# Optimization experiments

Hardware: AMD Instinct MI355X
Metric: run time of the kernel (lower is better)

The kernel has to match this reference:

```python
import jax, jax.numpy as jnp
import numpy as np

N_ORDER = 64
PRED_LEN = 720
SEQ_LEN = 720
ENC_IN = 321
BATCH = 16


def _hippo_legs(N):
    # HiPPO-LegS continuous transition (A, B), float64 numpy
    q = np.arange(N, dtype=np.float64)
    col, row = np.meshgrid(q, q)
    r = 2.0 * q + 1.0
    M = -(np.where(row >= col, r, 0.0) - np.diag(q))
    T = np.sqrt(np.diag(2.0 * q + 1.0))
    A = T @ M @ np.linalg.inv(T)
    B = np.diag(T)[:, None].copy()
    return A, B


def _discretize_bilinear(A, B, dt):
    # scipy.signal.cont2discrete(..., method='bilinear') equivalent
    N = A.shape[0]
    I = np.eye(N)
    BL = np.linalg.inv(I - (dt / 2.0) * A)
    Ad = BL @ (I + (dt / 2.0) * A)
    Bd = (BL @ (dt * B)).squeeze(-1)
    return Ad, Bd


def _legendre_eval_matrix(N, dt):
    # ss.eval_legendre(np.arange(N)[:,None], 1 - 2*vals).T via 3-term recurrence
    vals = np.arange(0.0, 1.0, dt)
    x = 1.0 - 2.0 * vals
    Ps = [np.ones_like(x), x]
    for n in range(1, N - 1):
        Ps.append(((2.0 * n + 1.0) * x * Ps[-1] - n * Ps[-2]) / (n + 1.0))
    return np.stack(Ps[:N], axis=0).T  # [len(vals), N]


def setup_inputs() -> dict:
    key = jax.random.key(0)
    k1, k2, k3 = jax.random.split(key, 3)
    dt = 1.0 / PRED_LEN
    A, B = _hippo_legs(N_ORDER)
    Ad, Bd = _discretize_bilinear(A, B, dt)
    eval_matrix = _legendre_eval_matrix(N_ORDER, dt)
    bound = 1.0 / np.sqrt(N_ORDER)  # torch nn.Linear default init range
    return {
        "x_enc": jax.random.normal(k1, (BATCH, SEQ_LEN, ENC_IN), dtype=jnp.float32),
        "A": jnp.asarray(Ad, dtype=jnp.float32),
        "B_vec": jnp.asarray(Bd, dtype=jnp.float32),
        "eval_matrix": jnp.asarray(eval_matrix, dtype=jnp.float32),
        "W_mlp": jax.random.uniform(k2, (N_ORDER, N_ORDER), jnp.float32, -bound, bound),
        "b_mlp": jax.random.uniform(k3, (N_ORDER,), jnp.float32, -bound, bound),
        "affine_weight": jnp.ones((1, 1, ENC_IN), jnp.float32),
        "affine_bias": jnp.zeros((1, 1, ENC_IN), jnp.float32),
    }


def reference(x_enc, A, B_vec, eval_matrix, W_mlp, b_mlp, affine_weight, affine_bias):
    P, N = eval_matrix.shape  # pred_len, proj_degree

    # RevIN-style instance normalization (means/stdev detached in torch)
    means = jax.lax.stop_gradient(jnp.mean(x_enc, axis=1, keepdims=True))
    x = x_enc - means
    stdev = jax.lax.stop_gradient(jnp.sqrt(jnp.var(x, axis=1, keepdims=True) + 1e-5))
    x = x / stdev
    x = x * affine_weight + affine_bias

    x_in = x[:, -P:]                         # [B, P, E]
    xs = jnp.transpose(x_in, (1, 0, 2))      # [P, B, E]: time-major for scan
    c0 = jnp.zeros((x_in.shape[0], x_in.shape[2], N), x_enc.dtype)

    def step(c, f):
        # c_t = c_{t-1} @ A^T + f_t B  (HiPPO-LegS linear recurrence)
        c_new = c @ A.T + f[..., None] * B_vec
        return c_new, c_new

    _, cs = jax.lax.scan(step, c0, xs)       # [P, B, E, N]

    out1 = cs @ W_mlp.T + b_mlp              # mlp over coefficient dim N
    x_dec_c = out1[P - 1]                    # [B, E, N] (seq_len >= pred_len branch)
    x_dec = x_dec_c @ eval_matrix.T          # [B, E, P] Legendre reconstruction
    x_dec = jnp.transpose(x_dec, (0, 2, 1))  # [B, P, E]

    # de-normalize
    x_dec = (x_dec - affine_bias) / (affine_weight + 1e-10)
    x_dec = x_dec * stdev + means
    return x_dec
```

## Files before the change

kernel.cpp:

```cpp
#include <hip/hip_runtime.h>
#include <math.h>

#define BATCH 16
#define SEQ   720
#define ENC   321
#define ENCP  324
#define NORD  64
#define PRED  720
#define NPAIR (BATCH*ENC)

#define WS_MEAN   0
#define WS_STDEV  (WS_MEAN + NPAIR)
#define WS_KT     (WS_STDEV + NPAIR)
#define WS_EWT    (WS_KT + PRED*NORD)
#define WS_EVB    (WS_EWT + NORD*PRED)
#define WS_C      (WS_EVB + PRED)
#define WS_A64    (WS_C + BATCH*NORD*ENCP)

#define GB_G      0
#define GB_PS_SUM 1572864
#define GB_PS_SS  (GB_PS_SUM + 24576)

__global__ __launch_bounds__(1024) void prep(const float* __restrict__ evalm,
        const float* __restrict__ W, const float* __restrict__ bm,
        const float* __restrict__ A, const float* __restrict__ Bv,
        float* __restrict__ ws)
{
    extern __shared__ float dsm[];
    const int tid  = threadIdx.x;
    const int lane = tid & 63;
    const int wv   = tid >> 6;
    if (blockIdx.x < 12) {
        float* smW = dsm;
        float* Et  = dsm + 64*65;
        const int r = blockIdx.x;
        for (int idx = tid; idx < 64*64; idx += 1024)
            smW[(idx>>6)*65 + (idx&63)] = W[idx];
        __syncthreads();
        float bv = bm[lane];
        #pragma unroll
        for (int k = 0; k < 4; k++) {
            int row = wv + k*16;
            if (row < 60) {
                int tp = r*60 + row;
                const float* ev = evalm + (size_t)tp*64;
                float acc = 0.f;
                #pragma unroll
                for (int kk = 0; kk < 16; kk++) {
                    float4 e4 = *(const float4*)&ev[4*kk];
                    acc += e4.x*smW[(4*kk+0)*65+lane] + e4.y*smW[(4*kk+1)*65+lane]
                         + e4.z*smW[(4*kk+2)*65+lane] + e4.w*smW[(4*kk+3)*65+lane];
                }
                Et[lane*61 + row] = acc;
                float pv = ev[lane] * bv;
                #pragma unroll
                for (int o = 32; o > 0; o >>= 1) pv += __shfl_down(pv, o);
                if (lane == 0) ws[WS_EVB + tp] = pv;
            }
        }
        __syncthreads();
        #pragma unroll
        for (int k = 0; k < 4; k++) {
            int idx = k*1024 + tid;
            int m = idx >> 6, row = idx & 63;
            if (row < 60)
                ws[WS_EWT + (size_t)m*720 + r*60 + row] = Et[m*61 + row];
        }
    } else {
        float* Kl  = dsm;
        float* Ap  = dsm + 4096;
        float* ApT = Ap + 64*68;
        float* Kt  = ws + WS_KT;
        for (int idx = tid; idx < 4096; idx += 1024) {
            int n = idx >> 6, m = idx & 63;
            float v = A[idx];
            Ap[n*68+m] = v; ApT[m*68+n] = v;
        }
        if (tid < 64) {
            float bv = Bv[tid];
            Kl[tid] = bv;
            Kt[(size_t)719*64 + tid] = bv;
        }
        __syncthreads();
        float ar[64];
        #pragma unroll
        for (int k = 0; k < 16; k++) {
            float4 v = *(const float4*)&Ap[lane*68 + 4*k];
            ar[4*k]=v.x; ar[4*k+1]=v.y; ar[4*k+2]=v.z; ar[4*k+3]=v.w;
        }
        for (int mm = 1; mm <= 32; mm <<= 1) {
            for (int j2 = mm + wv; j2 < 2*mm; j2 += 16) {
                const float* src = &Kl[(j2 - mm)*64];
                float acc = 0.f;
                #pragma unroll
                for (int k = 0; k < 16; k++) {
                    float4 s = *(const float4*)&src[4*k];
                    acc += ar[4*k]*s.x + ar[4*k+1]*s.y + ar[4*k+2]*s.z + ar[4*k+3]*s.w;
                }
                Kl[j2*64 + lane] = acc;
                Kt[(size_t)(719 - j2)*64 + lane] = acc;
            }
            float nacc[4];
            #pragma unroll
            for (int q = 0; q < 4; q++) {
                int c = wv*4 + q;
                const float* src = &ApT[c*68];
                float acc = 0.f;
                #pragma unroll
                for (int k = 0; k < 16; k++) {
                    float4 s = *(const float4*)&src[4*k];
                    acc += ar[4*k]*s.x + ar[4*k+1]*s.y + ar[4*k+2]*s.z + ar[4*k+3]*s.w;
                }
                nacc[q] = acc;
            }
            __syncthreads();
            #pragma unroll
            for (int q = 0; q < 4; q++) {
                int c = wv*4 + q;
                Ap[lane*68 + c]  = nacc[q];
                ApT[c*68 + lane] = nacc[q];
            }
            __syncthreads();
            #pragma unroll
            for (int k = 0; k < 16; k++) {
                float4 v = *(const float4*)&Ap[lane*68 + 4*k];
                ar[4*k]=v.x; ar[4*k+1]=v.y; ar[4*k+2]=v.z; ar[4*k+3]=v.w;
            }
        }
        for (int idx = tid; idx < 4096; idx += 1024)
            ws[WS_A64 + idx] = Ap[(idx>>6)*68 + (idx&63)];
    }
}

__global__ __launch_bounds__(256) void p2(float* __restrict__ ws)
{
    __shared__ float sv[4][64];
    const int lane = threadIdx.x & 63;
    const int wv   = threadIdx.x >> 6;
    const int r    = blockIdx.x*4 + wv;
    const float* A64 = ws + WS_A64;
    float* Kt = ws + WS_KT;
    float ar64[64];
    #pragma unroll
    for (int k = 0; k < 16; k++) {
        float4 v = *(const float4*)&A64[lane*64 + 4*k];
        ar64[4*k]=v.x; ar64[4*k+1]=v.y; ar64[4*k+2]=v.z; ar64[4*k+3]=v.w;
    }
    sv[wv][lane] = Kt[(size_t)(719 - r)*64 + lane];
    for (int j = r + 64; j <= 719; j += 64) {
        float acc = 0.f;
        #pragma unroll
        for (int k = 0; k < 16; k++) {
            float4 v = *(const float4*)&sv[wv][4*k];
            acc += ar64[4*k]*v.x + ar64[4*k+1]*v.y + ar64[4*k+2]*v.z + ar64[4*k+3]*v.w;
        }
        sv[wv][lane] = acc;
        Kt[(size_t)(719 - j)*64 + lane] = acc;
    }
}

__device__ inline float4 ldx(const float* __restrict__ x, int b, int t, int e4)
{
    float4 r = make_float4(0.f,0.f,0.f,0.f);
    const float* p = x + ((size_t)b*SEQ + t)*ENC;
    if (e4 + 3 < ENC) r = *(const float4*)&p[e4];
    else {
        if (e4   < ENC) r.x = p[e4];
        if (e4+1 < ENC) r.y = p[e4+1];
        if (e4+2 < ENC) r.z = p[e4+2];
    }
    return r;
}

__global__ __launch_bounds__(256) void k2(const float* __restrict__ x,
        float* __restrict__ gbuf, const float* __restrict__ ws)
{
    __shared__ float xt[2][12*64];
    __shared__ float ks[2][12*64];
    __shared__ float redn[12*64];
    __shared__ float reds[12*64];
    const int tid = threadIdx.x;
    const int bid = blockIdx.x;
    const int b = bid / 24, rem = bid % 24;
    const int et = rem / 4, tsp = rem % 4;
    const int e0 = et*64, t0 = tsp*180;

    const bool xon = tid < 192;
    const bool kon = tid >= 64;
    const int sx_t  = tid >> 4;
    const int sx_e4 = (tid & 15) * 4;
    const int sk    = tid - 64;
    const int sk_t  = sk >> 4;
    const int sk_m4 = (sk & 15) * 4;

    const float* Kt = ws + WS_KT;
    float s0=0,s1=0,s2=0,s3=0, q0=0,q1=0,q2=0,q3=0;
    float4 rx = make_float4(0,0,0,0), rk = make_float4(0,0,0,0);

    if (xon) rx = ldx(x, b, t0 + sx_t, e0 + sx_e4);
    if (kon) rk = *(const float4*)&Kt[(size_t)(t0 + sk_t)*64 + sk_m4];
    if (xon) {
        *(float4*)&xt[0][sx_t*64 + sx_e4] = rx;
        s0+=rx.x; s1+=rx.y; s2+=rx.z; s3+=rx.w;
        q0+=rx.x*rx.x; q1+=rx.y*rx.y; q2+=rx.z*rx.z; q3+=rx.w*rx.w;
    }
    if (kon) *(float4*)&ks[0][sk_t*64 + sk_m4] = rk;

    const int lane = tid & 63, wv = tid >> 6;
    const int mg = lane & 15, eg = lane >> 4;
    const int eoff = wv*16 + eg*4;
    float acc[4][4];
    #pragma unroll
    for (int j = 0; j < 4; j++)
        #pragma unroll
        for (int i = 0; i < 4; i++) acc[j][i] = 0.f;

    for (int ch = 0; ch < 15; ch++) {
        if (ch + 1 < 15) {
            if (xon) rx = ldx(x, b, t0 + (ch+1)*12 + sx_t, e0 + sx_e4);
            if (kon) rk = *(const float4*)&Kt[(size_t)(t0 + (ch+1)*12 + sk_t)*64 + sk_m4];
        }
        __syncthreads();
        const float* xb = xt[ch & 1];
        const float* kb = ks[ch & 1];
        #pragma unroll
        for (int tt = 0; tt < 12; tt++) {
            float4 f  = *(const float4*)&xb[tt*64 + eoff];
            float4 kv = *(const float4*)&kb[tt*64 + mg*4];
            acc[0][0]+=f.x*kv.x; acc[0][1]+=f.x*kv.y; acc[0][2]+=f.x*kv.z; acc[0][3]+=f.x*kv.w;
            acc[1][0]+=f.y*kv.x; acc[1][1]+=f.y*kv.y; acc[1][2]+=f.y*kv.z; acc[1][3]+=f.y*kv.w;
            acc[2][0]+=f.z*kv.x; acc[2][1]+=f.z*kv.y; acc[2][2]+=f.z*kv.z; acc[2][3]+=f.z*kv.w;
            acc[3][0]+=f.w*kv.x; acc[3][1]+=f.w*kv.y; acc[3][2]+=f.w*kv.z; acc[3][3]+=f.w*kv.w;
        }
        if (ch + 1 < 15) {
            if (xon) {
                *(float4*)&xt[(ch+1)&1][sx_t*64 + sx_e4] = rx;
                s0+=rx.x; s1+=rx.y; s2+=rx.z; s3+=rx.w;
                q0+=rx.x*rx.x; q1+=rx.y*rx.y; q2+=rx.z*rx.z; q3+=rx.w*rx.w;
            }
            if (kon) *(float4*)&ks[(ch+1)&1][sk_t*64 + sk_m4] = rk;
        }
    }

    float* g = gbuf + GB_G + (size_t)(tsp*96 + b*6 + et)*4096;
    #pragma unroll
    for (int j = 0; j < 4; j++)
        *(float4*)&g[(eoff + j)*64 + mg*4] = make_float4(acc[j][0], acc[j][1], acc[j][2], acc[j][3]);

    __syncthreads();
    if (xon) {
        redn[sx_t*64 + sx_e4+0] = s0; redn[sx_t*64 + sx_e4+1] = s1;
        redn[sx_t*64 + sx_e4+2] = s2; redn[sx_t*64 + sx_e4+3] = s3;
        reds[sx_t*64 + sx_e4+0] = q0; reds[sx_t*64 + sx_e4+1] = q1;
        reds[sx_t*64 + sx_e4+2] = q2; reds[sx_t*64 + sx_e4+3] = q3;
    }
    __syncthreads();
    if (tid < 64) {
        float s = 0.f, q = 0.f;
        #pragma unroll
        for (int rr = 0; rr < 12; rr++) { s += redn[rr*64 + tid]; q += reds[rr*64 + tid]; }
        const size_t o = (size_t)((tsp*16 + b)*6 + et)*64 + tid;
        gbuf[GB_PS_SUM + o] = s;
        gbuf[GB_PS_SS  + o] = q;
    }
}

__global__ __launch_bounds__(256) void k2b(const float* __restrict__ aw,
        const float* __restrict__ ab, const float* __restrict__ gbuf,
        float* __restrict__ ws)
{
    __shared__ float ssc[64], ssh[64], sksum[64];
    __shared__ float kred[4][64];
    __shared__ float T[64*65];
    const int tid = threadIdx.x;
    const int b = blockIdx.x / 6, et = blockIdx.x % 6;
    const int e0 = et*64;

    if (tid < 64) {
        float s = 0.f, q = 0.f;
        #pragma unroll
        for (int tsp = 0; tsp < 4; tsp++) {
            const size_t o = (size_t)((tsp*16 + b)*6 + et)*64 + tid;
            s += gbuf[GB_PS_SUM + o];
            q += gbuf[GB_PS_SS  + o];
        }
        float mean = s * (1.0f/SEQ);
        float var  = q * (1.0f/SEQ) - mean*mean;
        float sd   = sqrtf(var + 1e-5f);
        int e = e0 + tid;
        float a  = (e < ENC) ? aw[e] : 0.f;
        float av = (e < ENC) ? ab[e] : 0.f;
        float sc = a / sd;
        ssc[tid] = sc; ssh[tid] = av - mean*sc;
        if (e < ENC) {
            ws[WS_MEAN  + b*ENC + e] = mean;
            ws[WS_STDEV + b*ENC + e] = sd;
        }
    }
    {
        const int m = tid & 63, g = tid >> 6;
        const float* Kt = ws + WS_KT;
        float s = 0.f;
        for (int r = g*180; r < (g+1)*180; r++) s += Kt[(size_t)r*64 + m];
        kred[g][m] = s;
    }
    __syncthreads();
    if (tid < 64) sksum[tid] = kred[0][tid] + kred[1][tid] + kred[2][tid] + kred[3][tid];
    __syncthreads();

    const float* g0 = gbuf + GB_G + (size_t)(b*6 + et)*4096;
    #pragma unroll
    for (int k = 0; k < 16; k++) {
        int idx = k*256 + tid;
        int el = idx >> 6, m = idx & 63;
        float gs = g0[idx] + g0[(size_t)96*4096 + idx]
                 + g0[(size_t)192*4096 + idx] + g0[(size_t)288*4096 + idx];
        T[m*65 + el] = ssc[el]*gs + ssh[el]*sksum[m];
    }
    __syncthreads();
    float* C = ws + WS_C + (size_t)b*64*ENCP;
    #pragma unroll
    for (int k = 0; k < 16; k++) {
        int idx = k*256 + tid;
        int m = idx >> 6, el = idx & 63;
        int e = e0 + el;
        if (e < ENCP) C[(size_t)m*ENCP + e] = (e < ENC) ? T[m*65 + el] : 0.f;
    }
}

__global__ __launch_bounds__(256) void k3(const float* __restrict__ aw,
        const float* __restrict__ ab, const float* __restrict__ ws,
        float* __restrict__ out)
{
    __shared__ float EWm[64*68];
    __shared__ float Cm[64*132];
    const int tid = threadIdx.x;
    const int b   = blockIdx.x / 36;
    const int r   = blockIdx.x % 36;
    const int tt0 = (r / 3) * 64;
    const int e0  = (r % 3) * 128;

    const float* EWT = ws + WS_EWT;
    #pragma unroll
    for (int k = 0; k < 4; k++) {
        int slot = k*256 + tid;
        int m = slot >> 4, t4 = (slot & 15)*4;
        int tp = tt0 + t4;
        float4 v;
        if (tp + 3 < PRED) v = *(const float4*)&EWT[(size_t)m*720 + tp];
        else {
            v = make_float4(0.f,0.f,0.f,0.f);
            if (tp   < PRED) v.x = EWT[(size_t)m*720 + tp];
            if (tp+1 < PRED) v.y = EWT[(size_t)m*720 + tp+1];
            if (tp+2 < PRED) v.z = EWT[(size_t)m*720 + tp+2];
        }
        *(float4*)&EWm[m*68 + t4] = v;
    }
    const float* C = ws + WS_C + (size_t)b*64*ENCP;
    #pragma unroll
    for (int k = 0; k < 8; k++) {
        int slot = k*256 + tid;
        int m = slot >> 5, e4 = (slot & 31)*4;
        float4 v = make_float4(0.f,0.f,0.f,0.f);
        if (e0 + e4 + 3 < ENCP) v = *(const float4*)&C[(size_t)m*ENCP + e0 + e4];
        *(float4*)&Cm[m*132 + e4] = v;
    }
    __syncthreads();

    const int tx = tid & 31;
    const int ty = tid >> 5;
    float acc[8][4];
    #pragma unroll
    for (int i = 0; i < 8; i++)
        #pragma unroll
        for (int j = 0; j < 4; j++) acc[i][j] = 0.f;

    #pragma unroll 4
    for (int m = 0; m < 64; m++) {
        float4 c4 = *(const float4*)&Cm[m*132 + tx*4];
        float4 w0 = *(const float4*)&EWm[m*68 + ty*8];
        float4 w1 = *(const float4*)&EWm[m*68 + ty*8 + 4];
        acc[0][0]+=w0.x*c4.x; acc[0][1]+=w0.x*c4.y; acc[0][2]+=w0.x*c4.z; acc[0][3]+=w0.x*c4.w;
        acc[1][0]+=w0.y*c4.x; acc[1][1]+=w0.y*c4.y; acc[1][2]+=w0.y*c4.z; acc[1][3]+=w0.y*c4.w;
        acc[2][0]+=w0.z*c4.x; acc[2][1]+=w0.z*c4.y; acc[2][2]+=w0.z*c4.z; acc[2][3]+=w0.z*c4.w;
        acc[3][0]+=w0.w*c4.x; acc[3][1]+=w0.w*c4.y; acc[3][2]+=w0.w*c4.z; acc[3][3]+=w0.w*c4.w;
        acc[4][0]+=w1.x*c4.x; acc[4][1]+=w1.x*c4.y; acc[4][2]+=w1.x*c4.z; acc[4][3]+=w1.x*c4.w;
        acc[5][0]+=w1.y*c4.x; acc[5][1]+=w1.y*c4.y; acc[5][2]+=w1.y*c4.z; acc[5][3]+=w1.y*c4.w;
        acc[6][0]+=w1.z*c4.x; acc[6][1]+=w1.z*c4.y; acc[6][2]+=w1.z*c4.z; acc[6][3]+=w1.z*c4.w;
        acc[7][0]+=w1.w*c4.x; acc[7][1]+=w1.w*c4.y; acc[7][2]+=w1.w*c4.z; acc[7][3]+=w1.w*c4.w;
    }

    const int ebase = e0 + tx*4;
    float mean[4], sd[4], iaw[4], abe[4];
    #pragma unroll
    for (int j = 0; j < 4; j++) {
        int e = ebase + j;
        if (e < ENC) {
            int p = b*ENC + e;
            mean[j] = ws[WS_MEAN + p];
            sd[j]   = ws[WS_STDEV + p];
            iaw[j]  = 1.0f/(aw[e] + 1e-10f);
            abe[j]  = ab[e];
        } else { mean[j]=0.f; sd[j]=0.f; iaw[j]=0.f; abe[j]=0.f; }
    }
    const float* evb = ws + WS_EVB;
    #pragma unroll
    for (int i = 0; i < 8; i++) {
        int tp = tt0 + ty*8 + i;
        if (tp < PRED) {
            float ev = evb[tp];
            float* op = out + ((size_t)b*PRED + tp)*ENC;
            #pragma unroll
            for (int j = 0; j < 4; j++) {
                int e = ebase + j;
                if (e < ENC)
                    op[e] = (acc[i][j] + ev - abe[j]) * iaw[j] * sd[j] + mean[j];
            }
        }
    }
}

extern "C" void kernel_launch(void* const* d_in, const int* in_sizes, int n_in,
                              void* d_out, int out_size, void* d_ws, size_t ws_size,
                              hipStream_t stream)
{
    const float* x     = (const float*)d_in[0];
    const float* A     = (const float*)d_in[1];
    const float* Bv    = (const float*)d_in[2];
    const float* evalm = (const float*)d_in[3];
    const float* W     = (const float*)d_in[4];
    const float* bm    = (const float*)d_in[5];
    const float* aw    = (const float*)d_in[6];
    const float* ab    = (const float*)d_in[7];
    float* ws  = (float*)d_ws;
    float* out = (float*)d_out;

    const size_t smbytes = 12800 * sizeof(float);
    hipFuncSetAttribute((const void*)prep, hipFuncAttributeMaxDynamicSharedMemorySize, (int)smbytes);

    prep<<<13, 1024, smbytes, stream>>>(evalm, W, bm, A, Bv, ws);
    p2  <<<16, 256, 0, stream>>>(ws);
    k2  <<<BATCH*6*4, 256, 0, stream>>>(x, out, ws);
    k2b <<<BATCH*6, 256, 0, stream>>>(aw, ab, out, ws);
    k3  <<<576, 256, 0, stream>>>(aw, ab, ws, out);
}
```

Before: 159.5 us.

## Fuse prep stages and normalization into fewer kernels, cutting launches from five to three

The p2 kernel's 64-step Krylov extension is folded into the last prep block, which also computes the column sums of K directly. The k2b reduction/normalization stage is merged into a new k3f kernel that builds the scaled coefficient tile in shared memory and loops over three output time tiles per block. The intermediate G buffer moves from the output buffer into the workspace, its layout is transposed to suit the fused consumer, and the C/mean/stdev round trips are removed. In exchange, the Krylov tail now runs serially in one block of 16 waves, and k3f launches 192 blocks instead of 576, so there is less parallelism per launch.

```diff
diff --git a/kernel.cpp b/kernel.cpp
--- a/kernel.cpp
+++ b/kernel.cpp
@@ -4,37 +4,32 @@
 #define BATCH 16
 #define SEQ   720
 #define ENC   321
-#define ENCP  324
 #define NORD  64
 #define PRED  720
 #define NPAIR (BATCH*ENC)
 
-#define WS_MEAN   0
-#define WS_STDEV  (WS_MEAN + NPAIR)
-#define WS_KT     (WS_STDEV + NPAIR)
-#define WS_EWT    (WS_KT + PRED*NORD)
-#define WS_EVB    (WS_EWT + NORD*PRED)
-#define WS_C      (WS_EVB + PRED)
-#define WS_A64    (WS_C + BATCH*NORD*ENCP)
-
-#define GB_G      0
-#define GB_PS_SUM 1572864
-#define GB_PS_SS  (GB_PS_SUM + 24576)
+#define WS_KT    0
+#define WS_EWT   (WS_KT + PRED*NORD)
+#define WS_EVB   (WS_EWT + NORD*PRED)
+#define WS_KSUM  (WS_EVB + PRED)
+#define WS_G     (WS_KSUM + 64)
+#define WS_PSUM  (WS_G + 4*96*4096)
+#define WS_PSS   (WS_PSUM + 4*16*6*64)
 
 __global__ __launch_bounds__(1024) void prep(const float* __restrict__ evalm,
         const float* __restrict__ W, const float* __restrict__ bm,
         const float* __restrict__ A, const float* __restrict__ Bv,
         float* __restrict__ ws)
 {
-    extern __shared__ float dsm[];
+    __shared__ float dsm[12800];
     const int tid  = threadIdx.x;
     const int lane = tid & 63;
     const int wv   = tid >> 6;
     if (blockIdx.x < 12) {
         float* smW = dsm;
-        float* Et  = dsm + 64*65;
+        float* Et  = dsm + 4160;
         const int r = blockIdx.x;
-        for (int idx = tid; idx < 64*64; idx += 1024)
+        for (int idx = tid; idx < 4096; idx += 1024)
             smW[(idx>>6)*65 + (idx&63)] = W[idx];
         __syncthreads();
         float bv = bm[lane];
@@ -69,17 +64,19 @@
     } else {
         float* Kl  = dsm;
         float* Ap  = dsm + 4096;
-        float* ApT = Ap + 64*68;
+        float* ApT = dsm + 8448;
         float* Kt  = ws + WS_KT;
         for (int idx = tid; idx < 4096; idx += 1024) {
             int n = idx >> 6, m = idx & 63;
             float v = A[idx];
             Ap[n*68+m] = v; ApT[m*68+n] = v;
         }
+        float ksml = 0.f;
         if (tid < 64) {
             float bv = Bv[tid];
             Kl[tid] = bv;
             Kt[(size_t)719*64 + tid] = bv;
+            ksml += bv;
         }
         __syncthreads();
         float ar[64];
@@ -99,6 +96,7 @@
                 }
                 Kl[j2*64 + lane] = acc;
                 Kt[(size_t)(719 - j2)*64 + lane] = acc;
+                ksml += acc;
             }
             float nacc[4];
             #pragma unroll
@@ -127,35 +125,32 @@
                 ar[4*k]=v.x; ar[4*k+1]=v.y; ar[4*k+2]=v.z; ar[4*k+3]=v.w;
             }
         }
-        for (int idx = tid; idx < 4096; idx += 1024)
-            ws[WS_A64 + idx] = Ap[(idx>>6)*68 + (idx&63)];
-    }
-}
-
-__global__ __launch_bounds__(256) void p2(float* __restrict__ ws)
-{
-    __shared__ float sv[4][64];
-    const int lane = threadIdx.x & 63;
-    const int wv   = threadIdx.x >> 6;
-    const int r    = blockIdx.x*4 + wv;
-    const float* A64 = ws + WS_A64;
-    float* Kt = ws + WS_KT;
-    float ar64[64];
-    #pragma unroll
-    for (int k = 0; k < 16; k++) {
-        float4 v = *(const float4*)&A64[lane*64 + 4*k];
-        ar64[4*k]=v.x; ar64[4*k+1]=v.y; ar64[4*k+2]=v.z; ar64[4*k+3]=v.w;
-    }
-    sv[wv][lane] = Kt[(size_t)(719 - r)*64 + lane];
-    for (int j = r + 64; j <= 719; j += 64) {
-        float acc = 0.f;
-        #pragma unroll
-        for (int k = 0; k < 16; k++) {
-            float4 v = *(const float4*)&sv[wv][4*k];
-            acc += ar64[4*k]*v.x + ar64[4*k+1]*v.y + ar64[4*k+2]*v.z + ar64[4*k+3]*v.w;
-        }
-        sv[wv][lane] = acc;
-        Kt[(size_t)(719 - j)*64 + lane] = acc;
+        float* sv = &ApT[wv*68];
+        #pragma unroll
+        for (int c = 0; c < 4; c++) {
+            const int r = wv + 16*c;
+            sv[lane] = Kl[r*64 + lane];
+            for (int j = r + 64; j <= 719; j += 64) {
+                float acc = 0.f;
+                #pragma unroll
+                for (int k = 0; k < 16; k++) {
+                    float4 v = *(const float4*)&sv[4*k];
+                    acc += ar[4*k]*v.x + ar[4*k+1]*v.y + ar[4*k+2]*v.z + ar[4*k+3]*v.w;
+                }
+                sv[lane] = acc;
+                Kt[(size_t)(719 - j)*64 + lane] = acc;
+                ksml += acc;
+            }
+        }
+        __syncthreads();
+        Kl[wv*64 + lane] = ksml;
+        __syncthreads();
+        if (tid < 64) {
+            float s = 0.f;
+            #pragma unroll
+            for (int k = 0; k < 16; k++) s += Kl[k*64 + tid];
+            ws[WS_KSUM + tid] = s;
+        }
     }
 }
 
@@ -173,7 +168,7 @@
 }
 
 __global__ __launch_bounds__(256) void k2(const float* __restrict__ x,
-        float* __restrict__ gbuf, const float* __restrict__ ws)
+        float* __restrict__ ws)
 {
     __shared__ float xt[2][12*64];
     __shared__ float ks[2][12*64];
@@ -207,8 +202,8 @@
     if (kon) *(float4*)&ks[0][sk_t*64 + sk_m4] = rk;
 
     const int lane = tid & 63, wv = tid >> 6;
-    const int mg = lane & 15, eg = lane >> 4;
-    const int eoff = wv*16 + eg*4;
+    const int elg = lane & 15;
+    const int mgr = wv*4 + (lane >> 4);
     float acc[4][4];
     #pragma unroll
     for (int j = 0; j < 4; j++)
@@ -225,8 +220,8 @@
         const float* kb = ks[ch & 1];
         #pragma unroll
         for (int tt = 0; tt < 12; tt++) {
-            float4 f  = *(const float4*)&xb[tt*64 + eoff];
-            float4 kv = *(const float4*)&kb[tt*64 + mg*4];
+            float4 f  = *(const float4*)&xb[tt*64 + elg*4];
+            float4 kv = *(const float4*)&kb[tt*64 + mgr*4];
             acc[0][0]+=f.x*kv.x; acc[0][1]+=f.x*kv.y; acc[0][2]+=f.x*kv.z; acc[0][3]+=f.x*kv.w;
             acc[1][0]+=f.y*kv.x; acc[1][1]+=f.y*kv.y; acc[1][2]+=f.y*kv.z; acc[1][3]+=f.y*kv.w;
             acc[2][0]+=f.z*kv.x; acc[2][1]+=f.z*kv.y; acc[2][2]+=f.z*kv.z; acc[2][3]+=f.z*kv.w;
@@ -242,10 +237,11 @@
         }
     }
 
-    float* g = gbuf + GB_G + (size_t)(tsp*96 + b*6 + et)*4096;
+    float* g = ws + WS_G + (size_t)(tsp*96 + b*6 + et)*4096;
     #pragma unroll
-    for (int j = 0; j < 4; j++)
-        *(float4*)&g[(eoff + j)*64 + mg*4] = make_float4(acc[j][0], acc[j][1], acc[j][2], acc[j][3]);
+    for (int i = 0; i < 4; i++)
+        *(float4*)&g[(mgr*4 + i)*64 + elg*4] =
+            make_float4(acc[0][i], acc[1][i], acc[2][i], acc[3][i]);
 
     __syncthreads();
     if (xon) {
@@ -260,161 +256,134 @@
         #pragma unroll
         for (int rr = 0; rr < 12; rr++) { s += redn[rr*64 + tid]; q += reds[rr*64 + tid]; }
         const size_t o = (size_t)((tsp*16 + b)*6 + et)*64 + tid;
-        gbuf[GB_PS_SUM + o] = s;
-        gbuf[GB_PS_SS  + o] = q;
+        ws[WS_PSUM + o] = s;
+        ws[WS_PSS  + o] = q;
     }
 }
 
-__global__ __launch_bounds__(256) void k2b(const float* __restrict__ aw,
-        const float* __restrict__ ab, const float* __restrict__ gbuf,
-        float* __restrict__ ws)
+__global__ __launch_bounds__(256) void k3f(const float* __restrict__ aw,
+        const float* __restrict__ ab, const float* __restrict__ ws,
+        float* __restrict__ out)
 {
-    __shared__ float ssc[64], ssh[64], sksum[64];
-    __shared__ float kred[4][64];
-    __shared__ float T[64*65];
+    __shared__ float Cm[64*132];
+    __shared__ float EWm[64*68];
+    __shared__ float ssc[128], ssh[128], smean[128], ssd[128], siaw[128], sabe[128];
+    __shared__ float kss[64];
     const int tid = threadIdx.x;
-    const int b = blockIdx.x / 6, et = blockIdx.x % 6;
-    const int e0 = et*64;
-
-    if (tid < 64) {
+    const int b   = blockIdx.x / 12;
+    const int rr  = blockIdx.x % 12;
+    const int eT  = rr / 4;
+    const int tq  = rr % 4;
+    const int e0  = eT * 128;
+    const int et0 = eT * 2;
+
+    if (tid < 128) {
+        const int el = tid, e = e0 + el;
+        const int et = et0 + (el >> 6), eli = el & 63;
         float s = 0.f, q = 0.f;
         #pragma unroll
         for (int tsp = 0; tsp < 4; tsp++) {
-            const size_t o = (size_t)((tsp*16 + b)*6 + et)*64 + tid;
-            s += gbuf[GB_PS_SUM + o];
-            q += gbuf[GB_PS_SS  + o];
+            const size_t o = (size_t)((tsp*16 + b)*6 + et)*64 + eli;
+            s += ws[WS_PSUM + o];
+            q += ws[WS_PSS  + o];
         }
         float mean = s * (1.0f/SEQ);
         float var  = q * (1.0f/SEQ) - mean*mean;
         float sd   = sqrtf(var + 1e-5f);
-        int e = e0 + tid;
-        float a  = (e < ENC) ? aw[e] : 0.f;
-        float av = (e < ENC) ? ab[e] : 0.f;
-        float sc = a / sd;
-        ssc[tid] = sc; ssh[tid] = av - mean*sc;
         if (e < ENC) {
-            ws[WS_MEAN  + b*ENC + e] = mean;
-            ws[WS_STDEV + b*ENC + e] = sd;
-        }
-    }
-    {
-        const int m = tid & 63, g = tid >> 6;
-        const float* Kt = ws + WS_KT;
-        float s = 0.f;
-        for (int r = g*180; r < (g+1)*180; r++) s += Kt[(size_t)r*64 + m];
-        kred[g][m] = s;
-    }
+            float a = aw[e], av = ab[e];
+            float sc = a / sd;
+            ssc[el] = sc; ssh[el] = av - mean*sc;
+            smean[el] = mean; ssd[el] = sd;
+            siaw[el] = 1.0f/(a + 1e-10f); sabe[el] = av;
+        } else {
+            ssc[el]=0.f; ssh[el]=0.f; smean[el]=0.f; ssd[el]=0.f; siaw[el]=0.f; sabe[el]=0.f;
+        }
+    }
+    if (tid < 64) kss[tid] = ws[WS_KSUM + tid];
     __syncthreads();
-    if (tid < 64) sksum[tid] = kred[0][tid] + kred[1][tid] + kred[2][tid] + kred[3][tid];
-    __syncthreads();
-
-    const float* g0 = gbuf + GB_G + (size_t)(b*6 + et)*4096;
-    #pragma unroll
-    for (int k = 0; k < 16; k++) {
-        int idx = k*256 + tid;
-        int el = idx >> 6, m = idx & 63;
-        float gs = g0[idx] + g0[(size_t)96*4096 + idx]
-                 + g0[(size_t)192*4096 + idx] + g0[(size_t)288*4096 + idx];
-        T[m*65 + el] = ssc[el]*gs + ssh[el]*sksum[m];
-    }
-    __syncthreads();
-    float* C = ws + WS_C + (size_t)b*64*ENCP;
-    #pragma unroll
-    for (int k = 0; k < 16; k++) {
-        int idx = k*256 + tid;
-        int m = idx >> 6, el = idx & 63;
-        int e = e0 + el;
-        if (e < ENCP) C[(size_t)m*ENCP + e] = (e < ENC) ? T[m*65 + el] : 0.f;
-    }
-}
-
-__global__ __launch_bounds__(256) void k3(const float* __restrict__ aw,
-        const float* __restrict__ ab, const float* __restrict__ ws,
-        float* __restrict__ out)
-{
-    __shared__ float EWm[64*68];
-    __shared__ float Cm[64*132];
-    const int tid = threadIdx.x;
-    const int b   = blockIdx.x / 36;
-    const int r   = blockIdx.x % 36;
-    const int tt0 = (r / 3) * 64;
-    const int e0  = (r % 3) * 128;
-
-    const float* EWT = ws + WS_EWT;
-    #pragma unroll
-    for (int k = 0; k < 4; k++) {
-        int slot = k*256 + tid;
-        int m = slot >> 4, t4 = (slot & 15)*4;
-        int tp = tt0 + t4;
-        float4 v;
-        if (tp + 3 < PRED) v = *(const float4*)&EWT[(size_t)m*720 + tp];
-        else {
-            v = make_float4(0.f,0.f,0.f,0.f);
-            if (tp   < PRED) v.x = EWT[(size_t)m*720 + tp];
-            if (tp+1 < PRED) v.y = EWT[(size_t)m*720 + tp+1];
-            if (tp+2 < PRED) v.z = EWT[(size_t)m*720 + tp+2];
-        }
-        *(float4*)&EWm[m*68 + t4] = v;
-    }
-    const float* C = ws + WS_C + (size_t)b*64*ENCP;
+
+    const float* G = ws + WS_G;
     #pragma unroll
     for (int k = 0; k < 8; k++) {
         int slot = k*256 + tid;
-        int m = slot >> 5, e4 = (slot & 31)*4;
-        float4 v = make_float4(0.f,0.f,0.f,0.f);
-        if (e0 + e4 + 3 < ENCP) v = *(const float4*)&C[(size_t)m*ENCP + e0 + e4];
-        *(float4*)&Cm[m*132 + e4] = v;
+        int m = slot >> 5, el4 = (slot & 31) * 4;
+        int et = et0 + (el4 >> 6), eli4 = el4 & 63;
+        size_t base = (size_t)(b*6 + et)*4096 + m*64 + eli4;
+        float4 g0 = *(const float4*)&G[base];
+        float4 g1 = *(const float4*)&G[base + (size_t) 96*4096];
+        float4 g2 = *(const float4*)&G[base + (size_t)192*4096];
+        float4 g3 = *(const float4*)&G[base + (size_t)288*4096];
+        float km = kss[m];
+        float4 c;
+        c.x = ssc[el4+0]*(g0.x+g1.x+g2.x+g3.x) + ssh[el4+0]*km;
+        c.y = ssc[el4+1]*(g0.y+g1.y+g2.y+g3.y) + ssh[el4+1]*km;
+        c.z = ssc[el4+2]*(g0.z+g1.z+g2.z+g3.z) + ssh[el4+2]*km;
+        c.w = ssc[el4+3]*(g0.w+g1.w+g2.w+g3.w) + ssh[el4+3]*km;
+        *(float4*)&Cm[m*132 + el4] = c;
     }
     __syncthreads();
 
+    const float* EWT = ws + WS_EWT;
+    const float* evb = ws + WS_EVB;
     const int tx = tid & 31;
     const int ty = tid >> 5;
-    float acc[8][4];
-    #pragma unroll
-    for (int i = 0; i < 8; i++)
-        #pragma unroll
-        for (int j = 0; j < 4; j++) acc[i][j] = 0.f;
-
-    #pragma unroll 4
-    for (int m = 0; m < 64; m++) {
-        float4 c4 = *(const float4*)&Cm[m*132 + tx*4];
-        float4 w0 = *(const float4*)&EWm[m*68 + ty*8];
-        float4 w1 = *(const float4*)&EWm[m*68 + ty*8 + 4];
-        acc[0][0]+=w0.x*c4.x; acc[0][1]+=w0.x*c4.y; acc[0][2]+=w0.x*c4.z; acc[0][3]+=w0.x*c4.w;
-        acc[1][0]+=w0.y*c4.x; acc[1][1]+=w0.y*c4.y; acc[1][2]+=w0.y*c4.z; acc[1][3]+=w0.y*c4.w;
-        acc[2][0]+=w0.z*c4.x; acc[2][1]+=w0.z*c4.y; acc[2][2]+=w0.z*c4.z; acc[2][3]+=w0.z*c4.w;
-        acc[3][0]+=w0.w*c4.x; acc[3][1]+=w0.w*c4.y; acc[3][2]+=w0.w*c4.z; acc[3][3]+=w0.w*c4.w;
-        acc[4][0]+=w1.x*c4.x; acc[4][1]+=w1.x*c4.y; acc[4][2]+=w1.x*c4.z; acc[4][3]+=w1.x*c4.w;
-        acc[5][0]+=w1.y*c4.x; acc[5][1]+=w1.y*c4.y; acc[5][2]+=w1.y*c4.z; acc[5][3]+=w1.y*c4.w;
-        acc[6][0]+=w1.z*c4.x; acc[6][1]+=w1.z*c4.y; acc[6][2]+=w1.z*c4.z; acc[6][3]+=w1.z*c4.w;
-        acc[7][0]+=w1.w*c4.x; acc[7][1]+=w1.w*c4.y; acc[7][2]+=w1.w*c4.z; acc[7][3]+=w1.w*c4.w;
-    }
-
-    const int ebase = e0 + tx*4;
-    float mean[4], sd[4], iaw[4], abe[4];
-    #pragma unroll
-    for (int j = 0; j < 4; j++) {
-        int e = ebase + j;
-        if (e < ENC) {
-            int p = b*ENC + e;
-            mean[j] = ws[WS_MEAN + p];
-            sd[j]   = ws[WS_STDEV + p];
-            iaw[j]  = 1.0f/(aw[e] + 1e-10f);
-            abe[j]  = ab[e];
-        } else { mean[j]=0.f; sd[j]=0.f; iaw[j]=0.f; abe[j]=0.f; }
-    }
-    const float* evb = ws + WS_EVB;
-    #pragma unroll
-    for (int i = 0; i < 8; i++) {
-        int tp = tt0 + ty*8 + i;
-        if (tp < PRED) {
-            float ev = evb[tp];
-            float* op = out + ((size_t)b*PRED + tp)*ENC;
+    for (int ti = 0; ti < 3; ti++) {
+        const int tt0 = (tq*3 + ti) * 64;
+        if (ti > 0) __syncthreads();
+        #pragma unroll
+        for (int k = 0; k < 4; k++) {
+            int slot = k*256 + tid;
+            int m = slot >> 4, t4 = (slot & 15)*4;
+            int tp = tt0 + t4;
+            float4 v;
+            if (tp + 3 < PRED) v = *(const float4*)&EWT[(size_t)m*720 + tp];
+            else {
+                v = make_float4(0.f,0.f,0.f,0.f);
+                if (tp   < PRED) v.x = EWT[(size_t)m*720 + tp];
+                if (tp+1 < PRED) v.y = EWT[(size_t)m*720 + tp+1];
+                if (tp+2 < PRED) v.z = EWT[(size_t)m*720 + tp+2];
+            }
+            *(float4*)&EWm[m*68 + t4] = v;
+        }
+        __syncthreads();
+
+        float acc[8][4];
+        #pragma unroll
+        for (int i = 0; i < 8; i++)
             #pragma unroll
-            for (int j = 0; j < 4; j++) {
-                int e = ebase + j;
-                if (e < ENC)
-                    op[e] = (acc[i][j] + ev - abe[j]) * iaw[j] * sd[j] + mean[j];
+            for (int j = 0; j < 4; j++) acc[i][j] = 0.f;
+
+        #pragma unroll 4
+        for (int m = 0; m < 64; m++) {
+            float4 c4 = *(const float4*)&Cm[m*132 + tx*4];
+            float4 w0 = *(const float4*)&EWm[m*68 + ty*8];
+            float4 w1 = *(const float4*)&EWm[m*68 + ty*8 + 4];
+            acc[0][0]+=w0.x*c4.x; acc[0][1]+=w0.x*c4.y; acc[0][2]+=w0.x*c4.z; acc[0][3]+=w0.x*c4.w;
+            acc[1][0]+=w0.y*c4.x; acc[1][1]+=w0.y*c4.y; acc[1][2]+=w0.y*c4.z; acc[1][3]+=w0.y*c4.w;
+            acc[2][0]+=w0.z*c4.x; acc[2][1]+=w0.z*c4.y; acc[2][2]+=w0.z*c4.z; acc[2][3]+=w0.z*c4.w;
+            acc[3][0]+=w0.w*c4.x; acc[3][1]+=w0.w*c4.y; acc[3][2]+=w0.w*c4.z; acc[3][3]+=w0.w*c4.w;
+            acc[4][0]+=w1.x*c4.x; acc[4][1]+=w1.x*c4.y; acc[4][2]+=w1.x*c4.z; acc[4][3]+=w1.x*c4.w;
+            acc[5][0]+=w1.y*c4.x; acc[5][1]+=w1.y*c4.y; acc[5][2]+=w1.y*c4.z; acc[5][3]+=w1.y*c4.w;
+            acc[6][0]+=w1.z*c4.x; acc[6][1]+=w1.z*c4.y; acc[6][2]+=w1.z*c4.z; acc[6][3]+=w1.z*c4.w;
+            acc[7][0]+=w1.w*c4.x; acc[7][1]+=w1.w*c4.y; acc[7][2]+=w1.w*c4.z; acc[7][3]+=w1.w*c4.w;
+        }
+
+        const int elb = tx*4;
+        const int ebase = e0 + elb;
+        #pragma unroll
+        for (int i = 0; i < 8; i++) {
+            int tp = tt0 + ty*8 + i;
+            if (tp < PRED) {
+                float ev = evb[tp];
+                float* op = out + ((size_t)b*PRED + tp)*ENC;
+                #pragma unroll
+                for (int j = 0; j < 4; j++) {
+                    int e = ebase + j;
+                    if (e < ENC)
+                        op[e] = (acc[i][j] + ev - sabe[elb+j]) * siaw[elb+j] * ssd[elb+j]
+                                + smean[elb+j];
+                }
             }
         }
     }
@@ -435,12 +404,7 @@
     float* ws  = (float*)d_ws;
     float* out = (float*)d_out;
 
-    const size_t smbytes = 12800 * sizeof(float);
-    hipFuncSetAttribute((const void*)prep, hipFuncAttributeMaxDynamicSharedMemorySize, (int)smbytes);
-
-    prep<<<13, 1024, smbytes, stream>>>(evalm, W, bm, A, Bv, ws);
-    p2  <<<16, 256, 0, stream>>>(ws);
-    k2  <<<BATCH*6*4, 256, 0, stream>>>(x, out, ws);
-    k2b <<<BATCH*6, 256, 0, stream>>>(aw, ab, out, ws);
-    k3  <<<576, 256, 0, stream>>>(aw, ab, ws, out);
+    prep<<<13, 1024, 0, stream>>>(evalm, W, bm, A, Bv, ws);
+    k2  <<<BATCH*6*4, 256, 0, stream>>>(x, ws);
+    k3f <<<192, 256, 0, stream>>>(aw, ab, ws, out);
 }
```

Measured after the change: 187.2 us. 17.4% more time.
